# Kernel optimization log

Hardware: AMD Instinct MI355X
Metric: run time of the kernel (lower is better)

The kernel has to match this reference:

```python
import jax, jax.numpy as jnp
import numpy as np

N, E, B = 50000, 400000, 8
ND, ED, H, L = 32, 16, 128, 3

def setup_inputs() -> dict:
    key = jax.random.key(0)
    ks = jax.random.split(key, 32)
    s = 0.05
    inp = {
        'x': jax.random.normal(ks[0], (N, ND), jnp.float32),
        'edge_attr': jax.random.normal(ks[1], (E, ED), jnp.float32),
        'global_feature': jax.random.normal(ks[2], (B, 1), jnp.float32),
        'edge_index': jax.random.randint(ks[3], (2, E), 0, N, jnp.int64),
        'batch': jnp.sort(jax.random.randint(ks[4], (N,), 0, B, jnp.int64)),
        # embeddings
        'Wn': jax.random.normal(ks[5], (ND, H), jnp.float32) * s,
        'bn': jnp.zeros((H,), jnp.float32),
        'We': jax.random.normal(ks[6], (ED, H), jnp.float32) * s,
        'be': jnp.zeros((H,), jnp.float32),
        'Wg': jax.random.normal(ks[7], (1, H), jnp.float32) * s,
        'bg': jnp.zeros((H,), jnp.float32),
        # message-passing layers (stacked over L)
        'mW1': jax.random.normal(ks[8], (L, 3 * H, H), jnp.float32) * s,
        'mb1': jnp.zeros((L, H), jnp.float32),
        'mW2': jax.random.normal(ks[9], (L, H, H), jnp.float32) * s,
        'mb2': jnp.zeros((L, H), jnp.float32),
        'uW1': jax.random.normal(ks[10], (L, 2 * H, H), jnp.float32) * s,
        'ub1': jnp.zeros((L, H), jnp.float32),
        'uW2': jax.random.normal(ks[11], (L, H, H), jnp.float32) * s,
        'ub2': jnp.zeros((L, H), jnp.float32),
        # readout MLP
        'rW1': jax.random.normal(ks[12], (2 * H, H), jnp.float32) * s,
        'rb1': jnp.zeros((H,), jnp.float32),
        'rW2': jax.random.normal(ks[13], (H, H // 2), jnp.float32) * s,
        'rb2': jnp.zeros((H // 2,), jnp.float32),
        'rW3': jax.random.normal(ks[14], (H // 2, 1), jnp.float32) * s,
        'rb3': jnp.zeros((1,), jnp.float32),
    }
    return inp

def reference(x, edge_attr, global_feature, Wn, bn, We, be, Wg, bg,
              mW1, mb1, mW2, mb2, uW1, ub1, uW2, ub2,
              rW1, rb1, rW2, rb2, rW3, rb3, edge_index, batch):
    h = x @ Wn + bn                      # [N,H]
    e = edge_attr @ We + be              # [E,H]
    g = global_feature @ Wg + bg         # [B,H]
    src, dst = edge_index[0], edge_index[1]  # PyG: x_j=source, x_i=target, aggregate at target
    for l in range(L):
        m_in = jnp.concatenate([h[dst], h[src], e], axis=1)            # [E,3H]
        m = jax.nn.relu(m_in @ mW1[l] + mb1[l]) @ mW2[l] + mb2[l]       # [E,H]
        aggr = jax.ops.segment_sum(m, dst, num_segments=N)              # [N,H]
        u_in = jnp.concatenate([h, aggr], axis=1)                       # [N,2H]
        upd = jax.nn.relu(u_in @ uW1[l] + ub1[l]) @ uW2[l] + ub2[l]
        h = h + upd
    counts = jax.ops.segment_sum(jnp.ones((N,), h.dtype), batch, num_segments=B)
    pooled = jax.ops.segment_sum(h, batch, num_segments=B) / jnp.maximum(counts, 1.0)[:, None]
    final = jnp.concatenate([pooled, g], axis=1)                        # [B,2H]
    out = jax.nn.relu(final @ rW1 + rb1)
    out = jax.nn.relu(out @ rW2 + rb2)
    return out @ rW3 + rb3                                              # [B,1]
```

## Files before the change

kernel.cpp:

```cpp
#include <hip/hip_runtime.h>

#define NN 50000
#define NPAD 50048
#define NE 400000
#define NBATCH 8
#define NDIM 32
#define EDIM 16
#define H 128
#define NLAYERS 3
#define CHUNK_ELEMS 4096
#define NODE_CHUNKS 24
#define ZW_CHUNK 8192
#define NSB 196
#define ZEB 128

#define EMB_B 1563
#define DEG_B 1563
#define ZWB (NLAYERS * 8)
#define WEFB NLAYERS
#define WUB (NLAYERS * 257)
#define P1_B (EMB_B + DEG_B + ZWB + WEFB + WUB)
#define K2_B (NSB + NLAYERS + NLAYERS * NODE_CHUNKS)
#define ZDZS_B (NPAD / 64)
#define ZE_B (NE / ZEB)
#define ZZ_B (ZDZS_B + ZE_B)

typedef __attribute__((ext_vector_type(8))) __bf16 bf16x8;
typedef __attribute__((ext_vector_type(16))) float f32x16;
typedef __attribute__((ext_vector_type(8))) short short8;
typedef __attribute__((ext_vector_type(2))) float v2f;

__device__ __forceinline__ void block_sync_lds() {
  asm volatile("s_waitcnt lgkmcnt(0)\ns_barrier" ::: "memory");
}
__device__ __forceinline__ v2f bf2f(unsigned u) {
  v2f r;
  r.x = __uint_as_float(u << 16);
  r.y = __uint_as_float(u & 0xffff0000u);
  return r;
}

__global__ __launch_bounds__(256) void p1_kernel(
    const float* __restrict__ x, const float* __restrict__ Wn,
    const float* __restrict__ bn, __bf16* __restrict__ hb,
    const int* __restrict__ ei, int* __restrict__ deg,
    const float* __restrict__ mW1, __bf16* __restrict__ ZW,
    const float* __restrict__ mb1, const float* __restrict__ We,
    const float* __restrict__ be, float* __restrict__ Wef,
    float* __restrict__ bm, const float* __restrict__ uW1,
    const float* __restrict__ mW2, const float* __restrict__ mb2,
    float* __restrict__ Wu, float* __restrict__ va) {
  __shared__ __align__(16) float smem[NDIM * H + 32 * NDIM];
  int bi = blockIdx.x;
  int tid = threadIdx.x;
  if (bi < EMB_B) {
    float* Ws = smem;
    float* xs = smem + NDIM * H;
    int nbase = bi * 32;
    for (int f = tid; f < NDIM * H; f += 256) Ws[f] = Wn[f];
    for (int f = tid; f < 32 * NDIM; f += 256) {
      int gi = nbase * NDIM + f;
      xs[f] = (gi < NN * NDIM) ? x[gi] : 0.f;
    }
    __syncthreads();
    int j = tid & 127, g = tid >> 7;
    float b = bn[j];
    for (int nn = 0; nn < 16; ++nn) {
      int node = nbase + g * 16 + nn;
      if (node < NN) {
        float acc = b;
#pragma unroll
        for (int k = 0; k < NDIM; ++k)
          acc = fmaf(xs[(g * 16 + nn) * NDIM + k], Ws[k * H + j], acc);
        hb[(size_t)node * H + j] = (__bf16)acc;
      }
    }
  } else if (bi < EMB_B + DEG_B) {
    int e = (bi - EMB_B) * 256 + tid;
    if (e < NE) atomicAdd(&deg[ei[NE + e]], 1);
  } else if (bi < EMB_B + DEG_B + ZWB) {
    int bb = bi - EMB_B - DEG_B;
    int l = bb / 8;
    int c = bb % 8;
    const float* w1 = mW1 + (size_t)l * 384 * H;
    __bf16* dst = ZW + ((size_t)l * 8 + c) * ZW_CHUNK;
    for (int it = 0; it < 32; ++it) {
      int flat = it * 256 + tid;
      int j = flat & 7;
      int lane = (flat >> 3) & 63;
      int nt = (flat >> 9) & 7;
      int hilo = flat >> 12;
      int k = c * 16 + ((lane >> 5) << 3) + j;
      int n = nt * 32 + (lane & 31);
      float w = (n < 128) ? w1[(size_t)k * H + n]
                          : w1[(size_t)(128 + k) * H + (n - 128)];
      __bf16 hi = (__bf16)w;
      __bf16 lo = (__bf16)(w - (float)hi);
      dst[flat] = hilo ? lo : hi;
    }
  } else if (bi < EMB_B + DEG_B + ZWB + WEFB) {
    if (tid < 128) {
      int l = bi - (EMB_B + DEG_B + ZWB);
      int n = tid;
      const float* w1 = mW1 + (size_t)l * 384 * H;
      float acc[EDIM];
#pragma unroll
      for (int i = 0; i < EDIM; ++i) acc[i] = 0.f;
      float accb = 0.f;
      for (int c = 0; c < H; ++c) {
        float wv = w1[(size_t)(256 + c) * H + n];
        accb = fmaf(be[c], wv, accb);
#pragma unroll
        for (int i = 0; i < EDIM; ++i)
          acc[i] = fmaf(We[i * H + c], wv, acc[i]);
      }
#pragma unroll
      for (int i = 0; i < EDIM; ++i)
        Wef[((size_t)l * EDIM + i) * H + n] = acc[i];
      bm[l * H + n] = mb1[l * H + n] + accb;
    }
  } else {
    if (tid < 128) {
      int bb = bi - (EMB_B + DEG_B + ZWB + WEFB);
      int l = bb / 257;
      int r = bb % 257;
      int j = tid;
      const float* u1 = uW1 + (size_t)l * 256 * H;
      if (r < 128) {
        Wu[((size_t)l * 256 + r) * H + j] = u1[(size_t)r * H + j];
      } else if (r < 256) {
        int i = r - 128;
        const float* m2 = mW2 + ((size_t)l * H + i) * H;
        float s = 0.f;
        for (int c = 0; c < H; ++c)
          s = fmaf(m2[c], u1[(size_t)(128 + c) * H + j], s);
        Wu[((size_t)l * 256 + r) * H + j] = s;
      } else {
        float s = 0.f;
        for (int c = 0; c < H; ++c)
          s = fmaf(mb2[l * H + c], u1[(size_t)(128 + c) * H + j], s);
        va[l * H + j] = s;
      }
    }
  }
}

__global__ __launch_bounds__(256) void k2_kernel(
    const int* __restrict__ deg, int* __restrict__ bsum,
    const float* __restrict__ Wef, __bf16* __restrict__ WefS,
    const float* __restrict__ Wu, const float* __restrict__ uW2,
    __bf16* __restrict__ WnS) {
  __shared__ int ws[4];
  int bi = blockIdx.x;
  int tid = threadIdx.x;
  if (bi < NSB) {
    int i = bi * 256 + tid;
    int lane = tid & 63, wid = tid >> 6;
    int v = (i < NN) ? deg[i] : 0;
#pragma unroll
    for (int off = 32; off; off >>= 1) v += __shfl_down(v, off);
    if (lane == 0) ws[wid] = v;
    __syncthreads();
    if (tid == 0) bsum[bi] = ws[0] + ws[1] + ws[2] + ws[3];
  } else if (bi < NSB + NLAYERS) {
    int l = bi - NSB;
    int nt = tid >> 6, lane = tid & 63;
    int n = nt * 32 + (lane & 31);
    int half = lane >> 5;
    const float* wl = Wef + (size_t)l * EDIM * H;
    __bf16* dst = WefS + (size_t)l * CHUNK_ELEMS;
#pragma unroll
    for (int j = 0; j < 8; ++j) {
      int k = half * 8 + j;
      float w = wl[(size_t)k * H + n];
      __bf16 hi = (__bf16)w;
      __bf16 lo = (__bf16)(w - (float)hi);
      dst[((0 * 4 + nt) * 64 + lane) * 8 + j] = hi;
      dst[((1 * 4 + nt) * 64 + lane) * 8 + j] = lo;
    }
  } else {
    int idx = bi - NSB - NLAYERS;
    int l = idx / NODE_CHUNKS;
    int c = idx % NODE_CHUNKS;
    int nt = tid >> 6, lane = tid & 63;
    int n = nt * 32 + (lane & 31);
    int half = lane >> 5;
    __bf16* dst = WnS + ((size_t)l * NODE_CHUNKS + c) * CHUNK_ELEMS;
#pragma unroll
    for (int j = 0; j < 8; ++j) {
      float w;
      if (c < 16) {
        int k = c * 16 + half * 8 + j;
        w = Wu[((size_t)l * 256 + k) * H + n];
      } else {
        int k = (c - 16) * 16 + half * 8 + j;
        w = uW2[((size_t)l * H + k) * H + n];
      }
      __bf16 hi = (__bf16)w;
      __bf16 lo = (__bf16)(w - (float)hi);
      dst[((0 * 4 + nt) * 64 + lane) * 8 + j] = hi;
      dst[((1 * 4 + nt) * 64 + lane) * 8 + j] = lo;
    }
  }
}

__global__ __launch_bounds__(256) void scan2_kernel(const int* __restrict__ bsum,
                                                    int* __restrict__ boff) {
  __shared__ int s[256];
  int t = threadIdx.x;
  int v = (t < NSB) ? bsum[t] : 0;
  s[t] = v;
  __syncthreads();
  for (int off = 1; off < 256; off <<= 1) {
    int u = (t >= off) ? s[t - off] : 0;
    __syncthreads();
    s[t] += u;
    __syncthreads();
  }
  if (t < NSB) boff[t] = s[t] - v;
}

__global__ __launch_bounds__(256) void scan3_kernel(const int* __restrict__ deg,
                                                    const int* __restrict__ boff,
                                                    int* __restrict__ cursor) {
  __shared__ int wsum[4], woff[4];
  int i = blockIdx.x * 256 + threadIdx.x;
  int lane = threadIdx.x & 63, wid = threadIdx.x >> 6;
  int orig = (i < NN) ? deg[i] : 0;
  int v = orig;
#pragma unroll
  for (int off = 1; off < 64; off <<= 1) {
    int u = __shfl_up(v, off);
    if (lane >= off) v += u;
  }
  if (lane == 63) wsum[wid] = v;
  __syncthreads();
  if (threadIdx.x == 0) {
    int r = 0;
#pragma unroll
    for (int w = 0; w < 4; ++w) {
      woff[w] = r;
      r += wsum[w];
    }
  }
  __syncthreads();
  if (i < NN) cursor[i] = (v - orig) + woff[wid] + boff[blockIdx.x];
}

__global__ __launch_bounds__(256) void scatter_kernel(
    const int* __restrict__ ei, int* __restrict__ cursor,
    int2* __restrict__ seSrt) {
  int e = blockIdx.x * 256 + threadIdx.x;
  if (e < NE) {
    int d = ei[NE + e];
    int pos = atomicAdd(&cursor[d], 1);
    seSrt[pos] = make_int2(ei[e], e);
  }
}

__global__ __launch_bounds__(256) void gather_ea_kernel(
    const float* __restrict__ ea, const int2* __restrict__ seSrt,
    __bf16* __restrict__ eaSrt) {
  int fl = blockIdx.x * 256 + threadIdx.x;
  if (fl < NE) {
    int e = seSrt[fl].y;
    const float4* ep = (const float4*)(ea + (size_t)e * EDIM);
    __bf16* op = eaSrt + (size_t)fl * EDIM;
#pragma unroll
    for (int q = 0; q < 4; ++q) {
      float4 v = ep[q];
      op[q * 4 + 0] = (__bf16)v.x;
      op[q * 4 + 1] = (__bf16)v.y;
      op[q * 4 + 2] = (__bf16)v.z;
      op[q * 4 + 3] = (__bf16)v.w;
    }
  }
}

__global__ __launch_bounds__(256) void zz_kernel(
    const __bf16* __restrict__ hb, const __bf16* __restrict__ ZW,
    const float* __restrict__ bm, __bf16* __restrict__ z,
    const __bf16* __restrict__ eaSrt, const __bf16* __restrict__ WefS,
    __bf16* __restrict__ zePre) {
  __shared__ __align__(16) __bf16 Bt[2][ZW_CHUNK];
  int bi = blockIdx.x;
  int tid = threadIdx.x;
  int wid = tid >> 6, lane = tid & 63, m = lane & 31, half = lane >> 5;
  if (bi < ZDZS_B) {
    int rg = wid & 1;
    int nh = wid >> 1;
    int nb = bi * 64;
    int row = nb + rg * 32 + m;
    const __bf16* aH = hb + (size_t)row * H + half * 8;
    const short8* gW = (const short8*)ZW;
    short8* sB0 = (short8*)&Bt[0][0];
    short8* sB1 = (short8*)&Bt[1][0];
#pragma unroll
    for (int q = 0; q < 4; ++q) sB0[tid + q * 256] = gW[tid + q * 256];
    short8 p0 = gW[1024 + tid], p1 = gW[1024 + tid + 256];
    short8 p2 = gW[1024 + tid + 512], p3 = gW[1024 + tid + 768];
    f32x16 acc[4];
#pragma unroll
    for (int ntl = 0; ntl < 4; ++ntl)
#pragma unroll
      for (int r = 0; r < 16; ++r) acc[ntl][r] = 0.f;
    bf16x8 a = *(const bf16x8*)aH;
    block_sync_lds();

    for (int s = 0; s < 8; ++s) {
      int buf = s & 1;
      bf16x8 na = a;
      if (s + 1 < 8) na = *(const bf16x8*)(aH + (s + 1) * 16);
      if (s + 1 < 8) {
        short8* sb = buf ? sB0 : sB1;
        sb[tid] = p0;
        sb[tid + 256] = p1;
        sb[tid + 512] = p2;
        sb[tid + 768] = p3;
        if (s + 2 < 8) {
          p0 = gW[(size_t)(s + 2) * 1024 + tid];
          p1 = gW[(size_t)(s + 2) * 1024 + tid + 256];
          p2 = gW[(size_t)(s + 2) * 1024 + tid + 512];
          p3 = gW[(size_t)(s + 2) * 1024 + tid + 768];
        }
      }
      const __bf16* bb = &Bt[buf][0];
#pragma unroll
      for (int ntl = 0; ntl < 4; ++ntl) {
        int nt = nh * 4 + ntl;
        bf16x8 bh = *(const bf16x8*)&bb[((0 * 8 + nt) * 64 + lane) * 8];
        bf16x8 bl = *(const bf16x8*)&bb[((1 * 8 + nt) * 64 + lane) * 8];
        acc[ntl] = __builtin_amdgcn_mfma_f32_32x32x16_bf16(a, bh, acc[ntl], 0, 0, 0);
        acc[ntl] = __builtin_amdgcn_mfma_f32_32x32x16_bf16(a, bl, acc[ntl], 0, 0, 0);
      }
      a = na;
      if (s + 1 < 8) block_sync_lds();
    }

    float bmv[4];
#pragma unroll
    for (int ntl = 0; ntl < 4; ++ntl) {
      int nt = nh * 4 + ntl;
      bmv[ntl] = (nt < 4) ? bm[nt * 32 + m] : 0.f;
    }
#pragma unroll
    for (int ntl = 0; ntl < 4; ++ntl) {
      int nt = nh * 4 + ntl;
#pragma unroll
      for (int r = 0; r < 16; ++r) {
        int rowi = (r & 3) + 8 * (r >> 2) + 4 * half;
        z[(size_t)(nb + rg * 32 + rowi) * 256 + nt * 32 + m] =
            (__bf16)(acc[ntl][r] + bmv[ntl]);
      }
    }
  } else {
    __bf16* Bf = &Bt[0][0];
    ((short8*)Bf)[tid] = ((const short8*)WefS)[tid];
    ((short8*)Bf)[tid + 256] = ((const short8*)WefS)[tid + 256];
    int ebase = (bi - ZDZS_B) * ZEB + wid * 32;
    bf16x8 a = *(const bf16x8*)(eaSrt + (size_t)(ebase + m) * EDIM + half * 8);
    f32x16 acc[4];
#pragma unroll
    for (int nt = 0; nt < 4; ++nt)
#pragma unroll
      for (int r = 0; r < 16; ++r) acc[nt][r] = 0.f;
    block_sync_lds();
#pragma unroll
    for (int nt = 0; nt < 4; ++nt) {
      bf16x8 bh = *(const bf16x8*)&Bf[((0 * 4 + nt) * 64 + lane) * 8];
      bf16x8 bl = *(const bf16x8*)&Bf[((1 * 4 + nt) * 64 + lane) * 8];
      acc[nt] = __builtin_amdgcn_mfma_f32_32x32x16_bf16(a, bh, acc[nt], 0, 0, 0);
      acc[nt] = __builtin_amdgcn_mfma_f32_32x32x16_bf16(a, bl, acc[nt], 0, 0, 0);
    }
#pragma unroll
    for (int nt = 0; nt < 4; ++nt) {
#pragma unroll
      for (int r = 0; r < 16; ++r) {
        int rowi = (r & 3) + 8 * (r >> 2) + 4 * half;
        zePre[(size_t)(ebase + rowi) * H + nt * 32 + m] = (__bf16)acc[nt][r];
      }
    }
  }
}

__global__ __launch_bounds__(256) void edge_aggr_kernel(
    const __bf16* __restrict__ z, const int2* __restrict__ seSrt,
    const int* __restrict__ cend, const __bf16* __restrict__ zePre,
    __bf16* __restrict__ aggrB) {
  int node = blockIdx.x * 4 + (threadIdx.x >> 6);
  int lane = threadIdx.x & 63;
  int c0 = lane * 2;
  int end = cend[node];
  int start = node ? cend[node - 1] : 0;
  v2f acc = {0.f, 0.f};
  if (start < end) {
    v2f zd = bf2f(*(const unsigned*)(z + (size_t)node * 256 + c0));
    int sArr[4];
#pragma unroll
    for (int p = 0; p < 4; ++p)
      if (start + p < end) sArr[p] = seSrt[start + p].x;
    for (int e0 = start; e0 < end; e0 += 4) {
      unsigned zsb[4], zeb[4];
#pragma unroll
      for (int p = 0; p < 4; ++p) {
        if (e0 + p < end) {
          zsb[p] = *(const unsigned*)(z + (size_t)sArr[p] * 256 + 128 + c0);
          zeb[p] = *(const unsigned*)(zePre + (size_t)(e0 + p) * H + c0);
        }
      }
#pragma unroll
      for (int p = 0; p < 4; ++p)
        if (e0 + 4 + p < end) sArr[p] = seSrt[e0 + 4 + p].x;
#pragma unroll
      for (int p = 0; p < 4; ++p) {
        if (e0 + p < end) {
          v2f t = zd + bf2f(zsb[p]) + bf2f(zeb[p]);
          acc.x += fmaxf(t.x, 0.f);
          acc.y += fmaxf(t.y, 0.f);
        }
      }
    }
  }
  union { __bf16 b[2]; unsigned u; } pk;
  pk.b[0] = (__bf16)acc.x;
  pk.b[1] = (__bf16)acc.y;
  *(unsigned*)(aggrB + (size_t)node * H + c0) = pk.u;
}

__global__ __launch_bounds__(256) void node_update_mfma_kernel(
    __bf16* __restrict__ hb, const __bf16* __restrict__ aggrB,
    const int* __restrict__ deg, const __bf16* __restrict__ WnS,
    const float* __restrict__ ub1, const float* __restrict__ va,
    const float* __restrict__ ub2) {
  __shared__ __align__(16) __bf16 Bt[2][CHUNK_ELEMS];
  __shared__ __bf16 hid[2][32][132];
  __shared__ float degS[64];
  int tid = threadIdx.x;
  int nb = blockIdx.x * 64;
  if (tid < 64) degS[tid] = (float)deg[nb + tid];
  int wid = tid >> 6, lane = tid & 63, m = lane & 31, half = lane >> 5;
  int rg = wid & 1;
  int nh = wid >> 1;
  int row = nb + rg * 32 + m;
  const __bf16* aHb = hb + (size_t)row * H + half * 8;
  const __bf16* aGb = aggrB + (size_t)row * H + half * 8;
  const short8* gW = (const short8*)WnS;
  short8* sB0 = (short8*)&Bt[0][0];
  short8* sB1 = (short8*)&Bt[1][0];
  sB0[tid] = gW[tid];
  sB0[tid + 256] = gW[tid + 256];
  short8 p0 = gW[512 + tid], p1 = gW[512 + tid + 256];
  float bv1[2], bva[2];
#pragma unroll
  for (int ntl = 0; ntl < 2; ++ntl) {
    int nt = nh * 2 + ntl;
    bv1[ntl] = ub1[nt * 32 + m];
    bva[ntl] = va[nt * 32 + m];
  }
  f32x16 acc[2];
#pragma unroll
  for (int ntl = 0; ntl < 2; ++ntl)
#pragma unroll
    for (int r = 0; r < 16; ++r) acc[ntl][r] = 0.f;
  bf16x8 acur = *(const bf16x8*)aHb;
  block_sync_lds();

  for (int s = 0; s < 16; ++s) {
    int buf = s & 1;
    bf16x8 anext = acur;
    if (s + 1 < 16) {
      int sp = s + 1;
      anext = (sp < 8) ? *(const bf16x8*)(aHb + sp * 16)
                       : *(const bf16x8*)(aGb + (sp - 8) * 16);
    }
    {
      short8* sb = buf ? sB0 : sB1;
      sb[tid] = p0;
      sb[tid + 256] = p1;
      if (s + 2 < NODE_CHUNKS) {
        p0 = gW[(size_t)(s + 2) * 512 + tid];
        p1 = gW[(size_t)(s + 2) * 512 + tid + 256];
      }
    }
    const __bf16* bb = &Bt[buf][0];
#pragma unroll
    for (int ntl = 0; ntl < 2; ++ntl) {
      int nt = nh * 2 + ntl;
      bf16x8 bh = *(const bf16x8*)&bb[((0 * 4 + nt) * 64 + lane) * 8];
      bf16x8 bl = *(const bf16x8*)&bb[((1 * 4 + nt) * 64 + lane) * 8];
      acc[ntl] = __builtin_amdgcn_mfma_f32_32x32x16_bf16(acur, bh, acc[ntl], 0, 0, 0);
      acc[ntl] = __builtin_amdgcn_mfma_f32_32x32x16_bf16(acur, bl, acc[ntl], 0, 0, 0);
    }
    acur = anext;
    block_sync_lds();
  }

#pragma unroll
  for (int ntl = 0; ntl < 2; ++ntl) {
    int nt = nh * 2 + ntl;
#pragma unroll
    for (int r = 0; r < 16; ++r) {
      int rowi = (r & 3) + 8 * (r >> 2) + 4 * half;
      float v = acc[ntl][r] + bv1[ntl] + degS[rg * 32 + rowi] * bva[ntl];
      hid[rg][rowi][nt * 32 + m] = (__bf16)fmaxf(v, 0.f);
      acc[ntl][r] = 0.f;
    }
  }
  block_sync_lds();

  for (int s = 16; s < NODE_CHUNKS; ++s) {
    int buf = s & 1;
    if (s + 1 < NODE_CHUNKS) {
      short8* sb = buf ? sB0 : sB1;
      sb[tid] = p0;
      sb[tid + 256] = p1;
      if (s + 2 < NODE_CHUNKS) {
        p0 = gW[(size_t)(s + 2) * 512 + tid];
        p1 = gW[(size_t)(s + 2) * 512 + tid + 256];
      }
    }
    bf16x8 ah = *(const bf16x8*)&hid[rg][m][(s - 16) * 16 + half * 8];
    const __bf16* bb = &Bt[buf][0];
#pragma unroll
    for (int ntl = 0; ntl < 2; ++ntl) {
      int nt = nh * 2 + ntl;
      bf16x8 bh = *(const bf16x8*)&bb[((0 * 4 + nt) * 64 + lane) * 8];
      bf16x8 bl = *(const bf16x8*)&bb[((1 * 4 + nt) * 64 + lane) * 8];
      acc[ntl] = __builtin_amdgcn_mfma_f32_32x32x16_bf16(ah, bh, acc[ntl], 0, 0, 0);
      acc[ntl] = __builtin_amdgcn_mfma_f32_32x32x16_bf16(ah, bl, acc[ntl], 0, 0, 0);
    }
    if (s + 1 < NODE_CHUNKS) block_sync_lds();
  }

#pragma unroll
  for (int ntl = 0; ntl < 2; ++ntl) {
    int nt = nh * 2 + ntl;
    float b2 = ub2[nt * 32 + m];
#pragma unroll
    for (int r = 0; r < 16; ++r) {
      int rowi = (r & 3) + 8 * (r >> 2) + 4 * half;
      size_t idx = (size_t)(nb + rg * 32 + rowi) * H + nt * 32 + m;
      float hv = (float)hb[idx];
      hb[idx] = (__bf16)(hv + acc[ntl][r] + b2);
    }
  }
}

__global__ __launch_bounds__(256) void pool_kernel(
    const __bf16* __restrict__ hb, const int* __restrict__ batch,
    float* __restrict__ pooled, int* __restrict__ counts) {
  __shared__ float pS[NBATCH * H];
  __shared__ int cS[NBATCH];
  int tid = threadIdx.x;
  for (int i = tid; i < NBATCH * H; i += 256) pS[i] = 0.f;
  if (tid < NBATCH) cS[tid] = 0;
  __syncthreads();
  int c = tid & 15;
  int r0 = tid >> 4;
  int nbase = blockIdx.x * 128;
  v2f acc4[4] = {{0.f, 0.f}, {0.f, 0.f}, {0.f, 0.f}, {0.f, 0.f}};
  int cnt = 0;
  int cur = -1;
#pragma unroll
  for (int i = 0; i < 8; ++i) {
    int n = nbase + i * 16 + r0;
    if (n >= NN) break;
    int b = batch[n];
    if (b != cur) {
      if (cur >= 0) {
#pragma unroll
        for (int q = 0; q < 4; ++q) {
          atomicAdd(&pS[cur * H + c * 8 + q * 2], acc4[q].x);
          atomicAdd(&pS[cur * H + c * 8 + q * 2 + 1], acc4[q].y);
          acc4[q].x = 0.f;
          acc4[q].y = 0.f;
        }
        if (c == 0) atomicAdd(&cS[cur], cnt);
        cnt = 0;
      }
      cur = b;
    }
    uint4 v = *(const uint4*)(hb + (size_t)n * H + c * 8);
    acc4[0] += bf2f(v.x);
    acc4[1] += bf2f(v.y);
    acc4[2] += bf2f(v.z);
    acc4[3] += bf2f(v.w);
    cnt++;
  }
  if (cur >= 0) {
#pragma unroll
    for (int q = 0; q < 4; ++q) {
      atomicAdd(&pS[cur * H + c * 8 + q * 2], acc4[q].x);
      atomicAdd(&pS[cur * H + c * 8 + q * 2 + 1], acc4[q].y);
    }
    if (c == 0) atomicAdd(&cS[cur], cnt);
  }
  __syncthreads();
  for (int i = tid; i < NBATCH * H; i += 256) {
    float v = pS[i];
    if (v != 0.f) unsafeAtomicAdd(&pooled[i], v);
  }
  if (tid < NBATCH) {
    int cv = cS[tid];
    if (cv) atomicAdd(&counts[tid], cv);
  }
}

__global__ __launch_bounds__(128) void readout_kernel(
    const float* __restrict__ pooled, const int* __restrict__ counts,
    const float* __restrict__ gf, const float* __restrict__ Wg,
    const float* __restrict__ bg, const float* __restrict__ rW1,
    const float* __restrict__ rb1, const float* __restrict__ rW2,
    const float* __restrict__ rb2, const float* __restrict__ rW3,
    const float* __restrict__ rb3, float* __restrict__ out) {
  __shared__ float fin[256];
  __shared__ float t1[128];
  __shared__ float t2[64];
  int j = threadIdx.x;
  int b = blockIdx.x;
  float cnt = (float)counts[b];
  if (cnt < 1.f) cnt = 1.f;
  fin[j] = pooled[b * H + j] / cnt;
  fin[H + j] = fmaf(gf[b], Wg[j], bg[j]);
  __syncthreads();
  float a = rb1[j];
  for (int k = 0; k < 256; ++k) a = fmaf(fin[k], rW1[k * H + j], a);
  t1[j] = fmaxf(a, 0.f);
  __syncthreads();
  if (j < 64) {
    float a2 = rb2[j];
    for (int k = 0; k < 128; ++k) a2 = fmaf(t1[k], rW2[k * 64 + j], a2);
    t2[j] = fmaxf(a2, 0.f);
  }
  __syncthreads();
  if (j < 64) {
    float p = t2[j] * rW3[j];
#pragma unroll
    for (int off = 32; off; off >>= 1) p += __shfl_down(p, off);
    if (j == 0) out[b] = p + rb3[0];
  }
}

extern "C" void kernel_launch(void* const* d_in, const int* in_sizes, int n_in,
                              void* d_out, int out_size, void* d_ws, size_t ws_size,
                              hipStream_t stream) {
  const float* x   = (const float*)d_in[0];
  const float* ea  = (const float*)d_in[1];
  const float* gf  = (const float*)d_in[2];
  const int*   ei  = (const int*)d_in[3];
  const int*   bat = (const int*)d_in[4];
  const float* Wn  = (const float*)d_in[5];
  const float* bn  = (const float*)d_in[6];
  const float* We  = (const float*)d_in[7];
  const float* be  = (const float*)d_in[8];
  const float* Wg  = (const float*)d_in[9];
  const float* bg  = (const float*)d_in[10];
  const float* mW1 = (const float*)d_in[11];
  const float* mb1 = (const float*)d_in[12];
  const float* mW2 = (const float*)d_in[13];
  const float* mb2 = (const float*)d_in[14];
  const float* uW1 = (const float*)d_in[15];
  const float* ub1 = (const float*)d_in[16];
  const float* uW2 = (const float*)d_in[17];
  const float* ub2 = (const float*)d_in[18];
  const float* rW1 = (const float*)d_in[19];
  const float* rb1 = (const float*)d_in[20];
  const float* rW2 = (const float*)d_in[21];
  const float* rb2 = (const float*)d_in[22];
  const float* rW3 = (const float*)d_in[23];
  const float* rb3 = (const float*)d_in[24];

  char* p = (char*)d_ws;
  __bf16* hb     = (__bf16*)p; p += (size_t)NPAD * H * 2;
  __bf16* aggrB  = (__bf16*)p; p += (size_t)NPAD * H * 2;
  __bf16* z      = (__bf16*)p; p += (size_t)NPAD * 256 * 2;
  __bf16* zePre  = (__bf16*)p; p += (size_t)NE * H * 2;
  __bf16* eaSrt  = (__bf16*)p; p += (size_t)NE * EDIM * 2;
  int2*   seSrt  = (int2*)p;   p += (size_t)NE * 8;
  __bf16* ZW     = (__bf16*)p; p += (size_t)NLAYERS * 8 * ZW_CHUNK * 2;
  __bf16* WnS    = (__bf16*)p; p += (size_t)NLAYERS * NODE_CHUNKS * CHUNK_ELEMS * 2;
  __bf16* WefS   = (__bf16*)p; p += (size_t)NLAYERS * CHUNK_ELEMS * 2;
  float*  Wef    = (float*)p;  p += (size_t)NLAYERS * EDIM * H * 4;
  float*  bm     = (float*)p;  p += (size_t)NLAYERS * H * 4;
  float*  Wu     = (float*)p;  p += (size_t)NLAYERS * 256 * H * 4;
  float*  va     = (float*)p;  p += (size_t)NLAYERS * H * 4;
  int*    deg    = (int*)p;    p += (size_t)NPAD * 4;
  int*    cursor = (int*)p;    p += (size_t)NPAD * 4;
  int*    bsum   = (int*)p;    p += 256 * 4;
  int*    boff   = (int*)p;    p += 256 * 4;
  float*  pooled = (float*)p;  p += (size_t)NBATCH * H * 4;
  int*    counts = (int*)p;    p += 64;

  hipMemsetAsync(deg, 0, (size_t)NPAD * 4, stream);
  hipMemsetAsync(cursor, 0, (size_t)NPAD * 4, stream);
  hipMemsetAsync(pooled, 0, (size_t)NBATCH * H * 4, stream);
  hipMemsetAsync(counts, 0, 64, stream);

  p1_kernel<<<P1_B, 256, 0, stream>>>(x, Wn, bn, hb, ei, deg, mW1, ZW, mb1, We,
                                      be, Wef, bm, uW1, mW2, mb2, Wu, va);
  k2_kernel<<<K2_B, 256, 0, stream>>>(deg, bsum, Wef, WefS, Wu, uW2, WnS);
  scan2_kernel<<<1, 256, 0, stream>>>(bsum, boff);
  scan3_kernel<<<NSB, 256, 0, stream>>>(deg, boff, cursor);
  scatter_kernel<<<(NE + 255) / 256, 256, 0, stream>>>(ei, cursor, seSrt);
  gather_ea_kernel<<<(NE + 255) / 256, 256, 0, stream>>>(ea, seSrt, eaSrt);

  for (int l = 0; l < NLAYERS; ++l) {
    zz_kernel<<<ZZ_B, 256, 0, stream>>>(
        hb, ZW + (size_t)l * 8 * ZW_CHUNK, bm + (size_t)l * H, z,
        eaSrt, WefS + (size_t)l * CHUNK_ELEMS, zePre);
    edge_aggr_kernel<<<NPAD / 4, 256, 0, stream>>>(
        z, seSrt, cursor, zePre, aggrB);
    node_update_mfma_kernel<<<NPAD / 64, 256, 0, stream>>>(
        hb, aggrB, deg, WnS + (size_t)l * NODE_CHUNKS * CHUNK_ELEMS,
        ub1 + (size_t)l * H, va + (size_t)l * H, ub2 + (size_t)l * H);
  }

  pool_kernel<<<NPAD / 128, 256, 0, stream>>>(hb, bat, pooled, counts);
  readout_kernel<<<NBATCH, 128, 0, stream>>>(pooled, counts, gf, Wg, bg, rW1,
                                             rb1, rW2, rb2, rW3, rb3,
                                             (float*)d_out);
}
```

Baseline: 493.8 us.

## Fuse edge aggregation into node update kernel via shared memory

Removes the separate edge-aggregation kernel and its global aggr buffer. Each wave of the node-update kernel now gathers and sums the ReLU'd messages for 16 nodes itself, writing them into the shared hid buffer that the MFMA loop then reads as its A operand. This saves one launch per layer and a global write/read of the aggregate. The trade-off is much less parallelism for the latency-bound gather, since each wave walks 16 nodes one after another. The weight-preprocessing blocks are also reworked: We/be are staged in shared memory, loops are unrolled by four, and the Wu reduction is split across two half-blocks.

```diff
diff --git a/kernel.cpp b/kernel.cpp
--- a/kernel.cpp
+++ b/kernel.cpp
@@ -84,35 +84,58 @@
     int c = bb % 8;
     const float* w1 = mW1 + (size_t)l * 384 * H;
     __bf16* dst = ZW + ((size_t)l * 8 + c) * ZW_CHUNK;
-    for (int it = 0; it < 32; ++it) {
-      int flat = it * 256 + tid;
-      int j = flat & 7;
-      int lane = (flat >> 3) & 63;
-      int nt = (flat >> 9) & 7;
-      int hilo = flat >> 12;
-      int k = c * 16 + ((lane >> 5) << 3) + j;
-      int n = nt * 32 + (lane & 31);
-      float w = (n < 128) ? w1[(size_t)k * H + n]
+    for (int it = 0; it < 32; it += 4) {
+      float wv[4];
+#pragma unroll
+      for (int q = 0; q < 4; ++q) {
+        int flat = (it + q) * 256 + tid;
+        int j = flat & 7;
+        int lane = (flat >> 3) & 63;
+        int nt = (flat >> 9) & 7;
+        int k = c * 16 + ((lane >> 5) << 3) + j;
+        int n = nt * 32 + (lane & 31);
+        wv[q] = (n < 128) ? w1[(size_t)k * H + n]
                           : w1[(size_t)(128 + k) * H + (n - 128)];
-      __bf16 hi = (__bf16)w;
-      __bf16 lo = (__bf16)(w - (float)hi);
-      dst[flat] = hilo ? lo : hi;
+      }
+#pragma unroll
+      for (int q = 0; q < 4; ++q) {
+        int flat = (it + q) * 256 + tid;
+        int hilo = flat >> 12;
+        __bf16 hi = (__bf16)wv[q];
+        __bf16 lo = (__bf16)(wv[q] - (float)hi);
+        dst[flat] = hilo ? lo : hi;
+      }
     }
   } else if (bi < EMB_B + DEG_B + ZWB + WEFB) {
+    int l = bi - (EMB_B + DEG_B + ZWB);
+    float* WeS = smem;
+    float* beS = smem + 2048;
+    for (int f = tid; f < EDIM * H; f += 256) WeS[f] = We[f];
+    if (tid < 128) beS[tid] = be[tid];
+    __syncthreads();
     if (tid < 128) {
-      int l = bi - (EMB_B + DEG_B + ZWB);
       int n = tid;
-      const float* w1 = mW1 + (size_t)l * 384 * H;
+      const float* w1 = mW1 + (size_t)l * 384 * H + (size_t)256 * H + n;
       float acc[EDIM];
 #pragma unroll
       for (int i = 0; i < EDIM; ++i) acc[i] = 0.f;
       float accb = 0.f;
-      for (int c = 0; c < H; ++c) {
-        float wv = w1[(size_t)(256 + c) * H + n];
-        accb = fmaf(be[c], wv, accb);
-#pragma unroll
-        for (int i = 0; i < EDIM; ++i)
-          acc[i] = fmaf(We[i * H + c], wv, acc[i]);
+      for (int c = 0; c < H; c += 4) {
+        float w0 = w1[(size_t)(c + 0) * H];
+        float w1v = w1[(size_t)(c + 1) * H];
+        float w2 = w1[(size_t)(c + 2) * H];
+        float w3 = w1[(size_t)(c + 3) * H];
+        accb = fmaf(beS[c + 0], w0, accb);
+        accb = fmaf(beS[c + 1], w1v, accb);
+        accb = fmaf(beS[c + 2], w2, accb);
+        accb = fmaf(beS[c + 3], w3, accb);
+#pragma unroll
+        for (int i = 0; i < EDIM; ++i) {
+          acc[i] = fmaf(WeS[i * H + c + 0], w0, acc[i]);
+          acc[i] = fmaf(WeS[i * H + c + 1], w1v, acc[i]);
+          acc[i] = fmaf(WeS[i * H + c + 2], w2, acc[i]);
+          acc[i] = fmaf(WeS[i * H + c + 3], w3, acc[i]);
+        }
       }
 #pragma unroll
       for (int i = 0; i < EDIM; ++i)
@@ -120,26 +143,39 @@
       bm[l * H + n] = mb1[l * H + n] + accb;
     }
   } else {
-    if (tid < 128) {
-      int bb = bi - (EMB_B + DEG_B + ZWB + WEFB);
-      int l = bb / 257;
-      int r = bb % 257;
-      int j = tid;
-      const float* u1 = uW1 + (size_t)l * 256 * H;
-      if (r < 128) {
-        Wu[((size_t)l * 256 + r) * H + j] = u1[(size_t)r * H + j];
-      } else if (r < 256) {
-        int i = r - 128;
-        const float* m2 = mW2 + ((size_t)l * H + i) * H;
-        float s = 0.f;
-        for (int c = 0; c < H; ++c)
-          s = fmaf(m2[c], u1[(size_t)(128 + c) * H + j], s);
-        Wu[((size_t)l * 256 + r) * H + j] = s;
-      } else {
-        float s = 0.f;
-        for (int c = 0; c < H; ++c)
-          s = fmaf(mb2[l * H + c], u1[(size_t)(128 + c) * H + j], s);
-        va[l * H + j] = s;
+    int bb = bi - (EMB_B + DEG_B + ZWB + WEFB);
+    int l = bb / 257;
+    int r = bb % 257;
+    int j = tid & 127, hf = tid >> 7;
+    const float* u1 = uW1 + (size_t)l * 256 * H;
+    if (r < 128) {
+      if (tid < 128) Wu[((size_t)l * 256 + r) * H + j] = u1[(size_t)r * H + j];
+    } else {
+      float* rowS = smem;
+      float* redS = smem + 128;
+      if (tid < 128)
+        rowS[tid] = (r < 256) ? mW2[((size_t)l * H + (r - 128)) * H + tid]
+                              : mb2[l * H + tid];
+      __syncthreads();
+      int cb = hf * 64;
+      float s0 = 0.f, s1 = 0.f, s2 = 0.f, s3 = 0.f;
+      for (int c = 0; c < 64; c += 4) {
+        float a0 = u1[(size_t)(128 + cb + c + 0) * H + j];
+        float a1 = u1[(size_t)(128 + cb + c + 1) * H + j];
+        float a2 = u1[(size_t)(128 + cb + c + 2) * H + j];
+        float a3 = u1[(size_t)(128 + cb + c + 3) * H + j];
+        s0 = fmaf(rowS[cb + c + 0], a0, s0);
+        s1 = fmaf(rowS[cb + c + 1], a1, s1);
+        s2 = fmaf(rowS[cb + c + 2], a2, s2);
+        s3 = fmaf(rowS[cb + c + 3], a3, s3);
+      }
+      float s = (s0 + s1) + (s2 + s3);
+      if (hf == 1) redS[j] = s;
+      __syncthreads();
+      if (hf == 0) {
+        float tot = s + redS[j];
+        if (r < 256) Wu[((size_t)l * 256 + r) * H + j] = tot;
+        else va[l * H + j] = tot;
       }
     }
   }
@@ -383,55 +419,12 @@
   }
 }
 
-__global__ __launch_bounds__(256) void edge_aggr_kernel(
-    const __bf16* __restrict__ z, const int2* __restrict__ seSrt,
-    const int* __restrict__ cend, const __bf16* __restrict__ zePre,
-    __bf16* __restrict__ aggrB) {
-  int node = blockIdx.x * 4 + (threadIdx.x >> 6);
-  int lane = threadIdx.x & 63;
-  int c0 = lane * 2;
-  int end = cend[node];
-  int start = node ? cend[node - 1] : 0;
-  v2f acc = {0.f, 0.f};
-  if (start < end) {
-    v2f zd = bf2f(*(const unsigned*)(z + (size_t)node * 256 + c0));
-    int sArr[4];
-#pragma unroll
-    for (int p = 0; p < 4; ++p)
-      if (start + p < end) sArr[p] = seSrt[start + p].x;
-    for (int e0 = start; e0 < end; e0 += 4) {
-      unsigned zsb[4], zeb[4];
-#pragma unroll
-      for (int p = 0; p < 4; ++p) {
-        if (e0 + p < end) {
-          zsb[p] = *(const unsigned*)(z + (size_t)sArr[p] * 256 + 128 + c0);
-          zeb[p] = *(const unsigned*)(zePre + (size_t)(e0 + p) * H + c0);
-        }
-      }
-#pragma unroll
-      for (int p = 0; p < 4; ++p)
-        if (e0 + 4 + p < end) sArr[p] = seSrt[e0 + 4 + p].x;
-#pragma unroll
-      for (int p = 0; p < 4; ++p) {
-        if (e0 + p < end) {
-          v2f t = zd + bf2f(zsb[p]) + bf2f(zeb[p]);
-          acc.x += fmaxf(t.x, 0.f);
-          acc.y += fmaxf(t.y, 0.f);
-        }
-      }
-    }
-  }
-  union { __bf16 b[2]; unsigned u; } pk;
-  pk.b[0] = (__bf16)acc.x;
-  pk.b[1] = (__bf16)acc.y;
-  *(unsigned*)(aggrB + (size_t)node * H + c0) = pk.u;
-}
-
 __global__ __launch_bounds__(256) void node_update_mfma_kernel(
-    __bf16* __restrict__ hb, const __bf16* __restrict__ aggrB,
-    const int* __restrict__ deg, const __bf16* __restrict__ WnS,
-    const float* __restrict__ ub1, const float* __restrict__ va,
-    const float* __restrict__ ub2) {
+    __bf16* __restrict__ hb, const __bf16* __restrict__ z,
+    const int2* __restrict__ seSrt, const int* __restrict__ cend,
+    const __bf16* __restrict__ zePre, const int* __restrict__ deg,
+    const __bf16* __restrict__ WnS, const float* __restrict__ ub1,
+    const float* __restrict__ va, const float* __restrict__ ub2) {
   __shared__ __align__(16) __bf16 Bt[2][CHUNK_ELEMS];
   __shared__ __bf16 hid[2][32][132];
   __shared__ float degS[64];
@@ -439,11 +432,58 @@
   int nb = blockIdx.x * 64;
   if (tid < 64) degS[tid] = (float)deg[nb + tid];
   int wid = tid >> 6, lane = tid & 63, m = lane & 31, half = lane >> 5;
+  __bf16* aggrS = &hid[0][0][0];
+
+  {
+    int c0 = lane * 2;
+    int lr0 = wid * 16;
+    int node0 = nb + lr0;
+    int start = node0 ? cend[node0 - 1] : 0;
+    for (int k = 0; k < 16; ++k) {
+      int node = node0 + k;
+      int end = cend[node];
+      v2f acc2 = {0.f, 0.f};
+      if (start < end) {
+        v2f zd = bf2f(*(const unsigned*)(z + (size_t)node * 256 + c0));
+        int sArr[4];
+#pragma unroll
+        for (int p = 0; p < 4; ++p)
+          if (start + p < end) sArr[p] = seSrt[start + p].x;
+        for (int e0 = start; e0 < end; e0 += 4) {
+          unsigned zsb[4], zeb[4];
+#pragma unroll
+          for (int p = 0; p < 4; ++p) {
+            if (e0 + p < end) {
+              zsb[p] = *(const unsigned*)(z + (size_t)sArr[p] * 256 + 128 + c0);
+              zeb[p] = *(const unsigned*)(zePre + (size_t)(e0 + p) * H + c0);
+            }
+          }
+#pragma unroll
+          for (int p = 0; p < 4; ++p)
+            if (e0 + 4 + p < end) sArr[p] = seSrt[e0 + 4 + p].x;
+#pragma unroll
+          for (int p = 0; p < 4; ++p) {
+            if (e0 + p < end) {
+              v2f t = zd + bf2f(zsb[p]) + bf2f(zeb[p]);
+              acc2.x += fmaxf(t.x, 0.f);
+              acc2.y += fmaxf(t.y, 0.f);
+            }
+          }
+        }
+      }
+      union { __bf16 b[2]; unsigned u; } pk;
+      pk.b[0] = (__bf16)acc2.x;
+      pk.b[1] = (__bf16)acc2.y;
+      *(unsigned*)(aggrS + (size_t)(lr0 + k) * 132 + c0) = pk.u;
+      start = end;
+    }
+  }
+
   int rg = wid & 1;
   int nh = wid >> 1;
-  int row = nb + rg * 32 + m;
+  int lr = rg * 32 + m;
+  int row = nb + lr;
   const __bf16* aHb = hb + (size_t)row * H + half * 8;
-  const __bf16* aGb = aggrB + (size_t)row * H + half * 8;
   const short8* gW = (const short8*)WnS;
   short8* sB0 = (short8*)&Bt[0][0];
   short8* sB1 = (short8*)&Bt[1][0];
@@ -470,8 +510,10 @@
     bf16x8 anext = acur;
     if (s + 1 < 16) {
       int sp = s + 1;
-      anext = (sp < 8) ? *(const bf16x8*)(aHb + sp * 16)
-                       : *(const bf16x8*)(aGb + (sp - 8) * 16);
+      anext = (sp < 8)
+                  ? *(const bf16x8*)(aHb + sp * 16)
+                  : *(const bf16x8*)(aggrS + (size_t)lr * 132 +
+                                     (sp - 8) * 16 + half * 8);
     }
     {
       short8* sb = buf ? sB0 : sB1;
@@ -672,7 +714,6 @@
 
   char* p = (char*)d_ws;
   __bf16* hb     = (__bf16*)p; p += (size_t)NPAD * H * 2;
-  __bf16* aggrB  = (__bf16*)p; p += (size_t)NPAD * H * 2;
   __bf16* z      = (__bf16*)p; p += (size_t)NPAD * 256 * 2;
   __bf16* zePre  = (__bf16*)p; p += (size_t)NE * H * 2;
   __bf16* eaSrt  = (__bf16*)p; p += (size_t)NE * EDIM * 2;
@@ -708,10 +749,9 @@
     zz_kernel<<<ZZ_B, 256, 0, stream>>>(
         hb, ZW + (size_t)l * 8 * ZW_CHUNK, bm + (size_t)l * H, z,
         eaSrt, WefS + (size_t)l * CHUNK_ELEMS, zePre);
-    edge_aggr_kernel<<<NPAD / 4, 256, 0, stream>>>(
-        z, seSrt, cursor, zePre, aggrB);
     node_update_mfma_kernel<<<NPAD / 64, 256, 0, stream>>>(
-        hb, aggrB, deg, WnS + (size_t)l * NODE_CHUNKS * CHUNK_ELEMS,
+        hb, z, seSrt, cursor, zePre, deg,
+        WnS + (size_t)l * NODE_CHUNKS * CHUNK_ELEMS,
         ub1 + (size_t)l * H, va + (size_t)l * H, ub2 + (size_t)l * H);
   }
 
```

Measured after the change: 506.8 us. 1.03x slower.
